# Kernel optimization log

Measured on AMD Instinct MI355X. Metric: run time of the kernel, lower is better.

Reference implementation:

```python
import jax, jax.numpy as jnp
import numpy as np

DIM = 768
NUM_HEADS = 12
HEAD_DIM = DIM // NUM_HEADS
SCALE = HEAD_DIM ** -0.5


def setup_inputs() -> dict:
    key = jax.random.key(0)
    k1, k2, k3, k4 = jax.random.split(key, 4)
    x = jax.random.normal(k1, (8, 1024, DIM), dtype=jnp.float32)
    # torch Linear weights are [out, in]; no qkv bias (qkv_bias=False)
    qkv_w = jax.random.normal(k2, (3 * DIM, DIM), dtype=jnp.float32) * (DIM ** -0.5)
    proj_w = jax.random.normal(k3, (DIM, DIM), dtype=jnp.float32) * (DIM ** -0.5)
    proj_b = jax.random.normal(k4, (DIM,), dtype=jnp.float32) * 0.02
    return {"x": x, "qkv_w": qkv_w, "proj_w": proj_w, "proj_b": proj_b}


def reference(x, qkv_w, proj_w, proj_b):
    B, N, C = x.shape
    # qkv: [B, N, 3C] -> [3, B, H, N, D]
    qkv = jnp.einsum('bnc,oc->bno', x, qkv_w)
    qkv = qkv.reshape(B, N, 3, NUM_HEADS, HEAD_DIM).transpose(2, 0, 3, 1, 4)
    q, k, v = qkv[0], qkv[1], qkv[2]
    attn = jnp.einsum('bhnd,bhmd->bhnm', q, k) * SCALE
    attn = jax.nn.softmax(attn, axis=-1)
    out = jnp.einsum('bhnm,bhmd->bhnd', attn, v)  # [B, H, N, D]
    out = out.transpose(0, 2, 1, 3).reshape(B, N, C)
    out = jnp.einsum('bnc,oc->bno', out, proj_w) + proj_b
    return out
```

## Files before the change

### kernel.cpp

```cpp
#include <hip/hip_runtime.h>

typedef short bf16x8 __attribute__((ext_vector_type(8)));
typedef float f32x4 __attribute__((ext_vector_type(4)));
typedef float f32x16 __attribute__((ext_vector_type(16)));

#define AS1 __attribute__((address_space(1)))
#define AS3 __attribute__((address_space(3)))

__device__ __forceinline__ void gload16(const void* g, void* l) {
  __builtin_amdgcn_global_load_lds((const AS1 void*)g, (AS3 void*)l, 16, 0, 0);
}

__device__ __forceinline__ unsigned short f2bf(float f) {
  union { float f; unsigned u; } v; v.f = f;
  unsigned r = v.u + 0x7FFFu + ((v.u >> 16) & 1u);
  return (unsigned short)(r >> 16);
}

__device__ __forceinline__ unsigned cvtpk(float a, float b) {
  unsigned r;
  asm("v_cvt_pk_bf16_f32 %0, %1, %2" : "=v"(r) : "v"(a), "v"(b));
  return r;
}
__device__ __forceinline__ void plswap(unsigned& d, unsigned& s) {
  asm("v_permlane32_swap_b32 %0, %1" : "+v"(d), "+v"(s));
}

__global__ __launch_bounds__(256) void cast_all(
    const float* __restrict__ x, const float* __restrict__ w1, const float* __restrict__ w2,
    unsigned short* __restrict__ xb, unsigned short* __restrict__ w1b,
    unsigned short* __restrict__ w2b) {
  int i = blockIdx.x * blockDim.x + threadIdx.x;
  const float* in; unsigned short* out;
  if (i < 1572864) { in = x; out = xb; }
  else if (i < 2015232) { i -= 1572864; in = w1; out = w1b; }
  else { i -= 2015232; in = w2; out = w2b; }
  float4 v = reinterpret_cast<const float4*>(in)[i];
  ushort4 o; o.x = f2bf(v.x); o.y = f2bf(v.y); o.z = f2bf(v.z); o.w = f2bf(v.w);
  reinterpret_cast<ushort4*>(out)[i] = o;
}

template<int MODE>
__global__ __launch_bounds__(256) void gemm128(
    const unsigned short* __restrict__ A, const unsigned short* __restrict__ B,
    int K, int N,
    unsigned short* __restrict__ Qh, unsigned short* __restrict__ Kh,
    unsigned short* __restrict__ Vt,
    float* __restrict__ Cf, const float* __restrict__ bias) {
  constexpr int BM = (MODE == 0) ? 128 : 64;
  constexpr int MREP = BM / 32;
  __shared__ unsigned short Ab[BM * 64];
  __shared__ unsigned short Bb[128 * 64];
  const int tid = threadIdx.x, lane = tid & 63, wave = tid >> 6;
  const int l15 = lane & 15, lhi = lane >> 4;
  const int m0 = blockIdx.y * BM, n0 = blockIdx.x * 128;
  const int wr = wave >> 1, wc = wave & 1;

  f32x4 acc[MREP][4] = {};

  const int srow = tid >> 3;
  const int scol = (((tid & 7) * 16) ^ ((srow & 7) << 4)) >> 1;
  const unsigned short* aSrc = A + (size_t)(m0 + srow) * K + scol;
  const unsigned short* bSrc = B + (size_t)(n0 + srow) * K + scol;
  char* ldsA = (char*)Ab + wave * 1024;
  char* ldsB = (char*)Bb + wave * 1024;

  const int rswz = (l15 & 7) << 4;

  for (int k0 = 0; k0 < K; k0 += 64) {
    __syncthreads();
#pragma unroll
    for (int i = 0; i < BM / 32; ++i)
      gload16(aSrc + k0 + (size_t)32 * K * i, ldsA + i * 4096);
#pragma unroll
    for (int i = 0; i < 4; ++i)
      gload16(bSrc + k0 + (size_t)32 * K * i, ldsB + i * 4096);
    __syncthreads();
#pragma unroll
    for (int ks = 0; ks < 2; ++ks) {
      bf16x8 af[MREP], bfr[4];
#pragma unroll
      for (int mm = 0; mm < MREP; ++mm)
        af[mm] = *reinterpret_cast<const bf16x8*>(
            (char*)Ab + (wr * (BM / 2) + mm * 16 + l15) * 128 + ((ks * 64 + lhi * 16) ^ rswz));
#pragma unroll
      for (int nn = 0; nn < 4; ++nn)
        bfr[nn] = *reinterpret_cast<const bf16x8*>(
            (char*)Bb + (wc * 64 + nn * 16 + l15) * 128 + ((ks * 64 + lhi * 16) ^ rswz));
#pragma unroll
      for (int mm = 0; mm < MREP; ++mm)
#pragma unroll
        for (int nn = 0; nn < 4; ++nn)
          acc[mm][nn] = __builtin_amdgcn_mfma_f32_16x16x32_bf16(af[mm], bfr[nn], acc[mm][nn], 0, 0, 0);
    }
  }

  if (MODE == 0) {
    const int region = (n0 >= 1536) ? 2 : (n0 >= 768 ? 1 : 0);
    const float qs = (region == 0) ? 0.125f * 1.44269504088896340736f : 1.f;
#pragma unroll
    for (int mm = 0; mm < MREP; ++mm) {
      int gm = m0 + wr * (BM / 2) + mm * 16 + lhi * 4;
      int bb = gm >> 10, nb = gm & 1023;
#pragma unroll
      for (int nn = 0; nn < 4; ++nn) {
        int gn = n0 + wc * 64 + nn * 16 + l15 - region * 768;
        int d = gn & 63, hh = gn >> 6;
        if (region == 2) {
          ushort4 o;
          o.x = f2bf(acc[mm][nn][0]); o.y = f2bf(acc[mm][nn][1]);
          o.z = f2bf(acc[mm][nn][2]); o.w = f2bf(acc[mm][nn][3]);
          *reinterpret_cast<ushort4*>(&Vt[((size_t)(bb * 12 + hh) * 64 + d) * 1024 + nb]) = o;
        } else {
          unsigned short* dst =
              (region == 0 ? Qh : Kh) + ((size_t)(bb * 12 + hh) * 1024 + nb) * 64 + d;
#pragma unroll
          for (int r = 0; r < 4; ++r) dst[(size_t)r * 64] = f2bf(acc[mm][nn][r] * qs);
        }
      }
    }
  } else {
#pragma unroll
    for (int mm = 0; mm < MREP; ++mm) {
      int gm = m0 + wr * (BM / 2) + mm * 16 + lhi * 4;
#pragma unroll
      for (int nn = 0; nn < 4; ++nn) {
        int gn = n0 + wc * 64 + nn * 16 + l15;
        float bv = bias[gn];
#pragma unroll
        for (int r = 0; r < 4; ++r)
          Cf[(size_t)(gm + r) * N + gn] = acc[mm][nn][r] + bv;
      }
    }
  }
}

__global__ __launch_bounds__(256) void attn_kernel(
    const unsigned short* __restrict__ qh, const unsigned short* __restrict__ kh,
    const unsigned short* __restrict__ vt, unsigned short* __restrict__ aout) {
  __shared__ unsigned short KT[2][4096];
  __shared__ unsigned short VT[2][4096];

  const int tid = threadIdx.x, lane = tid & 63, wave = tid >> 6;
  const int l31 = lane & 31, hi = lane >> 5;
  const int bh = blockIdx.x % 96, qt = blockIdx.x / 96;
  const int b = bh / 12, h = bh % 12;

  const int srow = tid >> 3;
  const int scol = (((tid & 7) * 16) ^ ((srow & 7) << 4)) >> 1;
  const unsigned short* kS0 = kh + ((size_t)bh * 1024 + srow) * 64 + scol;
  const unsigned short* kS1 = kS0 + (size_t)32 * 64;
  const unsigned short* vS0 = vt + ((size_t)bh * 64 + srow) * 1024 + scol;
  const unsigned short* vS1 = vS0 + (size_t)32 * 1024;
  char* kD = (char*)&KT[0][0] + wave * 1024;
  char* vD = (char*)&VT[0][0] + wave * 1024;

  const int qw0 = qt * 128 + wave * 32;
  const unsigned short* qbase = qh + ((size_t)bh * 1024 + qw0 + l31) * 64 + hi * 8;
  bf16x8 qf[4];
#pragma unroll
  for (int ks = 0; ks < 4; ++ks)
    qf[ks] = *reinterpret_cast<const bf16x8*>(qbase + ks * 16);

  f32x16 oacc[2] = {};
  float lsum = 0.f;

  const int swz = (l31 & 7) << 4;
  const int rowb = l31 * 128;

  auto mkfrag = [&](const f32x16& e, int s8) -> bf16x8 {
    unsigned A0 = cvtpk(e[s8 + 0], e[s8 + 1]);
    unsigned A1 = cvtpk(e[s8 + 2], e[s8 + 3]);
    unsigned B0 = cvtpk(e[s8 + 4], e[s8 + 5]);
    unsigned B1 = cvtpk(e[s8 + 6], e[s8 + 7]);
    plswap(A0, B0);
    plswap(A1, B1);
    union { unsigned u[4]; bf16x8 v; } wu;
    wu.u[0] = A0; wu.u[1] = A1; wu.u[2] = B0; wu.u[3] = B1;
    return wu.v;
  };

  gload16(kS0, kD); gload16(kS1, kD + 4096);
  gload16(vS0, vD); gload16(vS1, vD + 4096);

  for (int kt = 0; kt < 16; ++kt) {
    const int cur = kt & 1;
    asm volatile("s_waitcnt vmcnt(0)" ::: "memory");
    __builtin_amdgcn_s_barrier();
    if (kt < 15) {
      const int kv = (kt + 1) * 64;
      char* kd = kD + (cur ^ 1) * 8192;
      char* vd = vD + (cur ^ 1) * 8192;
      gload16(kS0 + (size_t)kv * 64, kd); gload16(kS1 + (size_t)kv * 64, kd + 4096);
      gload16(vS0 + kv, vd); gload16(vS1 + kv, vd + 4096);
    }

    const char* kb = (const char*)&KT[cur][0];
    const char* vb = (const char*)&VT[cur][0];

    f32x16 p0 = {}, p1 = {};
    __builtin_amdgcn_s_setprio(1);
#pragma unroll
    for (int ks = 0; ks < 4; ++ks) {
      bf16x8 k0 = *reinterpret_cast<const bf16x8*>(kb + rowb + ((ks * 32 + hi * 16) ^ swz));
      bf16x8 k1 = *reinterpret_cast<const bf16x8*>(kb + 4096 + rowb + ((ks * 32 + hi * 16) ^ swz));
      p0 = __builtin_amdgcn_mfma_f32_32x32x16_bf16(k0, qf[ks], p0, 0, 0, 0);
      p1 = __builtin_amdgcn_mfma_f32_32x32x16_bf16(k1, qf[ks], p1, 0, 0, 0);
    }
    __builtin_amdgcn_s_setprio(0);

#pragma unroll
    for (int i = 0; i < 16; ++i) {
      p0[i] = __builtin_amdgcn_exp2f(p0[i]);
      p1[i] = __builtin_amdgcn_exp2f(p1[i]);
    }
    float su[8];
#pragma unroll
    for (int i = 0; i < 8; ++i)
      su[i] = (p0[i] + p0[i + 8]) + (p1[i] + p1[i + 8]);
    float s4[4];
#pragma unroll
    for (int i = 0; i < 4; ++i) s4[i] = su[i] + su[i + 4];
    lsum += (s4[0] + s4[1]) + (s4[2] + s4[3]);

    bf16x8 pb[4];
    pb[0] = mkfrag(p0, 0); pb[1] = mkfrag(p0, 8);
    pb[2] = mkfrag(p1, 0); pb[3] = mkfrag(p1, 8);

    __builtin_amdgcn_s_setprio(1);
#pragma unroll
    for (int kseg = 0; kseg < 4; ++kseg) {
      bf16x8 v0 = *reinterpret_cast<const bf16x8*>(vb + rowb + ((kseg * 32 + hi * 16) ^ swz));
      bf16x8 v1 = *reinterpret_cast<const bf16x8*>(vb + 4096 + rowb + ((kseg * 32 + hi * 16) ^ swz));
      oacc[0] = __builtin_amdgcn_mfma_f32_32x32x16_bf16(v0, pb[kseg], oacc[0], 0, 0, 0);
      oacc[1] = __builtin_amdgcn_mfma_f32_32x32x16_bf16(v1, pb[kseg], oacc[1], 0, 0, 0);
    }
    __builtin_amdgcn_s_setprio(0);
  }

  lsum += __shfl_xor(lsum, 32, 64);
  float inv = 1.f / lsum;
#pragma unroll
  for (int dblk = 0; dblk < 2; ++dblk)
#pragma unroll
    for (int g = 0; g < 4; ++g) {
      ushort4 o;
      o.x = f2bf(oacc[dblk][4 * g + 0] * inv);
      o.y = f2bf(oacc[dblk][4 * g + 1] * inv);
      o.z = f2bf(oacc[dblk][4 * g + 2] * inv);
      o.w = f2bf(oacc[dblk][4 * g + 3] * inv);
      int d = dblk * 32 + 8 * g + 4 * hi;
      *reinterpret_cast<ushort4*>(
          aout + ((size_t)(b * 1024 + qw0 + l31)) * 768 + h * 64 + d) = o;
    }
}

extern "C" void kernel_launch(void* const* d_in, const int* in_sizes, int n_in,
                              void* d_out, int out_size, void* d_ws, size_t ws_size,
                              hipStream_t stream) {
  const float* x      = (const float*)d_in[0];
  const float* qkv_w  = (const float*)d_in[1];
  const float* proj_w = (const float*)d_in[2];
  const float* proj_b = (const float*)d_in[3];
  float* out = (float*)d_out;

  char* ws = (char*)d_ws;
  unsigned short* xb     = (unsigned short*)(ws);
  unsigned short* wqkvb  = (unsigned short*)(ws + 12582912);
  unsigned short* wprojb = (unsigned short*)(ws + 16121856);
  unsigned short* qhb    = (unsigned short*)(ws + 17301504);
  unsigned short* khb    = (unsigned short*)(ws + 29884416);
  unsigned short* vtb    = (unsigned short*)(ws + 42467328);
  unsigned short* aob    = (unsigned short*)(ws + 55050240);

  cast_all<<<8448, 256, 0, stream>>>(x, qkv_w, proj_w, xb, wqkvb, wprojb);

  dim3 g1(2304 / 128, 8192 / 128);
  gemm128<0><<<g1, 256, 0, stream>>>(xb, wqkvb, 768, 2304, qhb, khb, vtb, nullptr, nullptr);

  attn_kernel<<<96 * 8, 256, 0, stream>>>(qhb, khb, vtb, aob);

  dim3 g2(768 / 128, 8192 / 64);
  gemm128<1><<<g2, 256, 0, stream>>>(aob, wprojb, 768, 768, nullptr, nullptr, nullptr, out, proj_b);
}
```

Baseline: 119.2 us.

## Triple-buffer attention K/V loads and remap GEMM blocks per XCD

The attention kernel moves from double to triple buffering of K/V tiles in LDS. It prefetches two tiles ahead and waits with vmcnt(4), so global loads overlap more compute. The GEMM launches become a 1D grid whose block ids are remapped so consecutive tiles land on the same XCD (bid&7 round-robin), aiming to improve L2 reuse of shared A/B rows. LDS use in attention grows by half, which may reduce occupancy.

```diff
diff --git a/kernel.cpp b/kernel.cpp
--- a/kernel.cpp
+++ b/kernel.cpp
@@ -25,6 +25,7 @@
 __device__ __forceinline__ void plswap(unsigned& d, unsigned& s) {
   asm("v_permlane32_swap_b32 %0, %1" : "+v"(d), "+v"(s));
 }
+
 
 __global__ __launch_bounds__(256) void cast_all(
     const float* __restrict__ x, const float* __restrict__ w1, const float* __restrict__ w2,
@@ -49,11 +50,15 @@
     float* __restrict__ Cf, const float* __restrict__ bias) {
   constexpr int BM = (MODE == 0) ? 128 : 64;
   constexpr int MREP = BM / 32;
+  constexpr int NX = (MODE == 0) ? 18 : 6;
+  constexpr int CPX = (MODE == 0) ? 144 : 96;
   __shared__ unsigned short Ab[BM * 64];
   __shared__ unsigned short Bb[128 * 64];
   const int tid = threadIdx.x, lane = tid & 63, wave = tid >> 6;
   const int l15 = lane & 15, lhi = lane >> 4;
-  const int m0 = blockIdx.y * BM, n0 = blockIdx.x * 128;
+  const int bid = blockIdx.x;
+  const int s = (bid & 7) * CPX + (bid >> 3);
+  const int m0 = (s / NX) * BM, n0 = (s % NX) * 128;
   const int wr = wave >> 1, wc = wave & 1;
 
   f32x4 acc[MREP][4] = {};
@@ -138,8 +143,8 @@
 __global__ __launch_bounds__(256) void attn_kernel(
     const unsigned short* __restrict__ qh, const unsigned short* __restrict__ kh,
     const unsigned short* __restrict__ vt, unsigned short* __restrict__ aout) {
-  __shared__ unsigned short KT[2][4096];
-  __shared__ unsigned short VT[2][4096];
+  __shared__ unsigned short KT[3][4096];
+  __shared__ unsigned short VT[3][4096];
 
   const int tid = threadIdx.x, lane = tid & 63, wave = tid >> 6;
   const int l31 = lane & 31, hi = lane >> 5;
@@ -152,8 +157,8 @@
   const unsigned short* kS1 = kS0 + (size_t)32 * 64;
   const unsigned short* vS0 = vt + ((size_t)bh * 64 + srow) * 1024 + scol;
   const unsigned short* vS1 = vS0 + (size_t)32 * 1024;
-  char* kD = (char*)&KT[0][0] + wave * 1024;
-  char* vD = (char*)&VT[0][0] + wave * 1024;
+  char* kDb = (char*)&KT[0][0] + wave * 1024;
+  char* vDb = (char*)&VT[0][0] + wave * 1024;
 
   const int qw0 = qt * 128 + wave * 32;
   const unsigned short* qbase = qh + ((size_t)bh * 1024 + qw0 + l31) * 64 + hi * 8;
@@ -180,17 +185,28 @@
     return wu.v;
   };
 
-  gload16(kS0, kD); gload16(kS1, kD + 4096);
-  gload16(vS0, vD); gload16(vS1, vD + 4096);
+#pragma unroll
+  for (int t = 0; t < 2; ++t) {
+    const int kv = t * 64;
+    char* kd = kDb + t * 8192;
+    char* vd = vDb + t * 8192;
+    gload16(kS0 + (size_t)kv * 64, kd); gload16(kS1 + (size_t)kv * 64, kd + 4096);
+    gload16(vS0 + kv, vd); gload16(vS1 + kv, vd + 4096);
+  }
 
   for (int kt = 0; kt < 16; ++kt) {
-    const int cur = kt & 1;
-    asm volatile("s_waitcnt vmcnt(0)" ::: "memory");
+    const int cur = kt % 3;
+    if (kt < 15) {
+      asm volatile("s_waitcnt vmcnt(4)" ::: "memory");
+    } else {
+      asm volatile("s_waitcnt vmcnt(0)" ::: "memory");
+    }
     __builtin_amdgcn_s_barrier();
-    if (kt < 15) {
-      const int kv = (kt + 1) * 64;
-      char* kd = kD + (cur ^ 1) * 8192;
-      char* vd = vD + (cur ^ 1) * 8192;
+    if (kt + 2 <= 15) {
+      const int kv = (kt + 2) * 64;
+      const int nb = (kt + 2) % 3;
+      char* kd = kDb + nb * 8192;
+      char* vd = vDb + nb * 8192;
       gload16(kS0 + (size_t)kv * 64, kd); gload16(kS1 + (size_t)kv * 64, kd + 4096);
       gload16(vS0 + kv, vd); gload16(vS1 + kv, vd + 4096);
     }
@@ -275,11 +291,9 @@
 
   cast_all<<<8448, 256, 0, stream>>>(x, qkv_w, proj_w, xb, wqkvb, wprojb);
 
-  dim3 g1(2304 / 128, 8192 / 128);
-  gemm128<0><<<g1, 256, 0, stream>>>(xb, wqkvb, 768, 2304, qhb, khb, vtb, nullptr, nullptr);
+  gemm128<0><<<1152, 256, 0, stream>>>(xb, wqkvb, 768, 2304, qhb, khb, vtb, nullptr, nullptr);
 
   attn_kernel<<<96 * 8, 256, 0, stream>>>(qhb, khb, vtb, aob);
 
-  dim3 g2(768 / 128, 8192 / 64);
-  gemm128<1><<<g2, 256, 0, stream>>>(aob, wprojb, 768, 768, nullptr, nullptr, nullptr, out, proj_b);
-}
+  gemm128<1><<<768, 256, 0, stream>>>(aob, wprojb, 768, 768, nullptr, nullptr, nullptr, out, proj_b);
+}
```

Measured after the change: 115.9 us. 2.7% less time.
